# Kernel tuning notes

Hardware: AMD Instinct MI355X
Metric: run time of the kernel (lower is better)

The kernel has to match this reference:

```python
import jax, jax.numpy as jnp
import numpy as np

BUFFER_C = 1.25

def setup_inputs() -> dict:
    key = jax.random.key(0)
    k1, k2, k3 = jax.random.split(key, 3)
    T, D, E = 4096, 1024, 8
    x = jax.random.normal(k1, (T, D), dtype=jnp.float32)
    Wg = jax.random.normal(k2, (D, E), dtype=jnp.float32) / np.sqrt(D)
    bg = jnp.zeros((E,), dtype=jnp.float32)
    W = jax.random.normal(k3, (E, D, D), dtype=jnp.float32) / np.sqrt(D)
    b = jnp.zeros((E, D), dtype=jnp.float32)
    return {"x": x, "Wg": Wg, "bg": bg, "W": W, "b": b}


def reference(x, Wg, bg, W, b):
    # Top-1 (Switch-style) routing with capacity buffer, per-expert Linear,
    # prob-weighted combine, plus load-balancing aux loss.
    T, D = x.shape
    E = W.shape[0]
    capacity = int(BUFFER_C * T / E)

    logits = x @ Wg + bg                      # [T, E]
    probs = jax.nn.softmax(logits, axis=-1)   # [T, E]
    top_idx = jnp.argmax(probs, axis=-1)      # [T]
    top_prob = jnp.take_along_axis(probs, top_idx[:, None], axis=-1)[:, 0]

    onehot = jax.nn.one_hot(top_idx, E, dtype=x.dtype)       # [T, E]
    # 1-indexed position of each token within its expert's buffer
    pos = jnp.cumsum(onehot, axis=0) * onehot                # [T, E]
    dispatch = jnp.where((onehot > 0) & (pos <= capacity), 1.0, 0.0).astype(x.dtype)

    # dense dispatch/combine equivalent of the masked per-expert loop
    xe = jnp.einsum('te,td->etd', dispatch, x)               # [E, T, D]
    ye = jnp.einsum('etd,edf->etf', xe, W) + b[:, None, :]   # [E, T, D]
    y = jnp.einsum('te,etf->tf', dispatch, ye)               # [T, D] (0 for dropped)
    out = y * top_prob[:, None]

    # aux load-balance loss: E * sum_e f_e * P_e
    f = onehot.mean(axis=0)
    P = probs.mean(axis=0)
    aux_loss = E * jnp.sum(f * P)
    return out, aux_loss
```

## Files before the change

### kernel.cpp

```cpp
#include <hip/hip_runtime.h>
#include <hip/hip_bf16.h>
#include <cstdint>

#define T_TOK 4096
#define D_DIM 1024
#define E_EXP 8
#define CAP   640
#define MAXDROP 3456
#define MT    10
#define GBLK  1024
#define NSUB  32

typedef __attribute__((ext_vector_type(8))) short short8;
typedef __attribute__((ext_vector_type(4))) float f32x4;

__device__ inline unsigned short f2bf(float f) {
    uint32_t u = __float_as_uint(f);
    u += 0x7fffu + ((u >> 16) & 1u);
    return (unsigned short)(u >> 16);
}

__device__ inline void dma16(const void* g, void* l) {
    __builtin_amdgcn_global_load_lds(
        (const __attribute__((address_space(1))) unsigned int*)g,
        (__attribute__((address_space(3))) unsigned int*)l, 16, 0, 0);
}

#define WB_TILE(e, nt, kt) ((((size_t)(e) * 16 + (nt)) * 16 + (kt)) * 4096)
#define XG_TILE(e, mt, kt) ((((size_t)(e) * MT + (mt)) * 16 + (kt)) * 4096)

__global__ __launch_bounds__(256) void prep_kernel(
    const float* __restrict__ x, const float* __restrict__ Wg,
    const float* __restrict__ bg, const float* __restrict__ W,
    unsigned short* __restrict__ Wb,
    int* __restrict__ top_idx, float* __restrict__ top_prob,
    float* __restrict__ blkpart)
{
    int bid = blockIdx.x;
    int tid = threadIdx.x;

    if (bid >= GBLK) {
        int bid2 = (bid - GBLK) * 2;
        int e   = bid2 >> 8;
        int kt  = (bid2 >> 4) & 15;
        int ntA = bid2 & 15;
        int k0  = kt * 64;
        const float* Wsrc = W + (size_t)e * D_DIM * D_DIM + (size_t)k0 * D_DIM;

        int c0 = tid, c1 = tid + 256;
        int g0 = c0 >> 6, n0c = c0 & 63;
        int g1 = c1 >> 6, n1c = c1 & 63;

        #pragma unroll
        for (int half = 0; half < 2; half++) {
            int n0 = (ntA + half) * 64;
            unsigned short* dst = Wb + WB_TILE(e, ntA + half, kt);
            const float* s0 = Wsrc + (size_t)(g0 * 8) * D_DIM + n0 + n0c;
            const float* s1 = Wsrc + (size_t)(g1 * 8) * D_DIM + n0 + n1c;
            float v[8], u[8];
            #pragma unroll
            for (int z = 0; z < 8; z++) v[z] = s0[(size_t)z * D_DIM];
            #pragma unroll
            for (int z = 0; z < 8; z++) u[z] = s1[(size_t)z * D_DIM];
            short8 a, b2;
            #pragma unroll
            for (int z = 0; z < 8; z++) { a[z] = (short)f2bf(v[z]); b2[z] = (short)f2bf(u[z]); }
            *(short8*)&dst[(size_t)c0 * 8] = a;
            *(short8*)&dst[(size_t)c1 * 8] = b2;
        }
    } else {
        __shared__ float probs_sm[4][8];
        int wid  = tid >> 6;
        int lane = tid & 63;
        int t = bid * 4 + wid;

        const float* xr = x + (size_t)t * D_DIM;

        float acc[8];
        #pragma unroll
        for (int e = 0; e < 8; e++) acc[e] = 0.f;

        #pragma unroll
        for (int ii = 0; ii < 16; ii++) {
            int d = lane + 64 * ii;
            float xv = xr[d];
            const float4* wr = (const float4*)(Wg + (size_t)d * 8);
            float4 a = wr[0], bq = wr[1];
            acc[0] += xv * a.x;  acc[1] += xv * a.y;
            acc[2] += xv * a.z;  acc[3] += xv * a.w;
            acc[4] += xv * bq.x; acc[5] += xv * bq.y;
            acc[6] += xv * bq.z; acc[7] += xv * bq.w;
        }
        #pragma unroll
        for (int off = 32; off > 0; off >>= 1) {
            #pragma unroll
            for (int e = 0; e < 8; e++) acc[e] += __shfl_xor(acc[e], off, 64);
        }
        if (lane == 0) {
            float lg[8];
            #pragma unroll
            for (int e = 0; e < 8; e++) lg[e] = acc[e] + bg[e];
            float m = lg[0]; int am = 0;
            #pragma unroll
            for (int e = 1; e < 8; e++) { if (lg[e] > m) { m = lg[e]; am = e; } }
            float ex[8], s = 0.f;
            #pragma unroll
            for (int e = 0; e < 8; e++) { ex[e] = __expf(lg[e] - m); s += ex[e]; }
            float inv = 1.f / s;
            top_idx[t]  = am;
            top_prob[t] = ex[am] * inv;
            #pragma unroll
            for (int e = 0; e < 8; e++) probs_sm[wid][e] = ex[e] * inv;
        }
        __syncthreads();
        if (tid < 8) {
            float s = probs_sm[0][tid] + probs_sm[1][tid]
                    + probs_sm[2][tid] + probs_sm[3][tid];
            blkpart[(size_t)bid * 8 + tid] = s;
        }
    }
}

__global__ __launch_bounds__(1024) void scan_kernel(
    const int* __restrict__ top_idx,
    int* __restrict__ tok_list, int* __restrict__ cnt,
    const float* __restrict__ blkpart,
    float* __restrict__ out, float* __restrict__ out_aux)
{
    __shared__ int counts[64][8];
    __shared__ int excl[64][8];
    __shared__ int fulltot[8];
    __shared__ int droplist[MAXDROP];
    __shared__ int ndrop;
    __shared__ float wpart[16][8];

    int tid  = threadIdx.x;
    int wv   = tid >> 6;
    int lane = tid & 63;
    unsigned long long ltmask = (lane == 0) ? 0ull : ((~0ull) >> (64 - lane));

    if (tid == 0) ndrop = 0;

    float p[8];
    {
        const float4* bp = (const float4*)(blkpart + (size_t)tid * 8);
        float4 p0 = bp[0], p1 = bp[1];
        p[0] = p0.x; p[1] = p0.y; p[2] = p0.z; p[3] = p0.w;
        p[4] = p1.x; p[5] = p1.y; p[6] = p1.z; p[7] = p1.w;
    }

    int ecache[4];
    #pragma unroll
    for (int c = 0; c < 4; c++)
        ecache[c] = top_idx[(4 * wv + c) * 64 + lane];

    #pragma unroll
    for (int c = 0; c < 4; c++) {
        int chunk = 4 * wv + c;
        int e = ecache[c];
        #pragma unroll
        for (int q = 0; q < 8; q++) {
            unsigned long long mk = __ballot(e == q);
            int tot = __popcll(mk);
            if (lane == q) counts[chunk][q] = tot;
        }
    }
    __syncthreads();

    if (wv == 0) {
        #pragma unroll
        for (int q = 0; q < 8; q++) {
            int v = counts[lane][q];
            int orig = v;
            #pragma unroll
            for (int off = 1; off < 64; off <<= 1) {
                int n = __shfl_up(v, off, 64);
                if (lane >= off) v += n;
            }
            excl[lane][q] = v - orig;
            int total = __shfl(v, 63, 64);
            if (lane == 0) {
                fulltot[q] = total;
                cnt[q] = total < CAP ? total : CAP;
            }
        }
    }
    __syncthreads();

    #pragma unroll
    for (int c = 0; c < 4; c++) {
        int chunk = 4 * wv + c;
        int t = chunk * 64 + lane;
        int e = ecache[c];
        int pos = 0;
        #pragma unroll
        for (int q = 0; q < 8; q++) {
            unsigned long long mk = __ballot(e == q);
            if (e == q) pos = excl[chunk][q] + __popcll(mk & ltmask);
        }
        if (pos < CAP) {
            tok_list[e * CAP + pos] = t;
        } else {
            int di = atomicAdd(&ndrop, 1);
            droplist[di] = t;
        }
    }

    #pragma unroll
    for (int off = 32; off > 0; off >>= 1) {
        #pragma unroll
        for (int e = 0; e < 8; e++) p[e] += __shfl_xor(p[e], off, 64);
    }
    if (lane == 0) {
        #pragma unroll
        for (int e = 0; e < 8; e++) wpart[wv][e] = p[e];
    }
    __syncthreads();

    int nd = ndrop;
    int grp = tid >> 8;
    int col = (tid & 255) * 4;
    float4 z = {0.f, 0.f, 0.f, 0.f};
    for (int d = grp; d < nd; d += 4) {
        int row = droplist[d];
        *(float4*)&out[(size_t)row * D_DIM + col] = z;
    }

    if (tid == 0) {
        float s = 0.f;
        #pragma unroll
        for (int e = 0; e < 8; e++) {
            float Pe = 0.f;
            #pragma unroll
            for (int w = 0; w < 16; w++) Pe += wpart[w][e];
            s += ((float)fulltot[e] / (float)T_TOK) * (Pe / (float)T_TOK);
        }
        out_aux[0] = (float)E_EXP * s;
    }
}

__global__ __launch_bounds__(256) void gather_kernel(
    const float* __restrict__ x, const int* __restrict__ tok_list,
    const int* __restrict__ cnt, unsigned short* __restrict__ xg)
{
    int bid = blockIdx.x;
    int e   = bid / (MT * 16);
    int rem = bid % (MT * 16);
    int mt  = rem >> 4, kt = rem & 15;
    int count = cnt[e];
    int m0 = mt * 64;
    if (m0 >= count) return;

    int tid = threadIdx.x;
    const int* tl = tok_list + e * CAP;
    unsigned short* dst = xg + XG_TILE(e, mt, kt);

    #pragma unroll
    for (int p = 0; p < 2; p++) {
        int c = tid + 256 * p;
        int g = c >> 6, row = c & 63;
        int gm = m0 + row;
        int tok = tl[gm < count ? gm : count - 1];
        const float* src = x + (size_t)tok * D_DIM + kt * 64 + g * 8;
        float4 v0 = *(const float4*)(src);
        float4 v1 = *(const float4*)(src + 4);
        short8 v;
        v[0] = f2bf(v0.x); v[1] = f2bf(v0.y); v[2] = f2bf(v0.z); v[3] = f2bf(v0.w);
        v[4] = f2bf(v1.x); v[5] = f2bf(v1.y); v[6] = f2bf(v1.z); v[7] = f2bf(v1.w);
        *(short8*)&dst[(size_t)c * 8] = v;
    }
}

__global__ __launch_bounds__(512) void expert_gemm(
    const unsigned short* __restrict__ xg, const unsigned short* __restrict__ Wb,
    const float* __restrict__ bias,
    const int* __restrict__ tok_list, const int* __restrict__ cnt,
    const float* __restrict__ top_prob, float* __restrict__ out)
{
    int orig = blockIdx.x;
    int bid  = (orig & 7) * 40 + (orig >> 3);
    int e   = bid / 40;
    int rem = bid % 40;
    int mtb = rem >> 3, ntb = rem & 7;
    int count = cnt[e];
    int m0 = mtb * 128;
    if (m0 >= count) return;
    int n0 = ntb * 128;

    __shared__ unsigned short Ab[3][2][4][64][8];
    __shared__ unsigned short Bb[3][2][4][64][8];

    int tid  = threadIdx.x;
    int lane = tid & 63, w = tid >> 6;
    int quad = lane >> 4, l16 = lane & 15;
    int wr = w >> 2, wc = w & 3;

    const int* tl = tok_list + e * CAP;

    int  wa    = w & 3;
    int  shalf = wa >> 1;
    int  sg0   = (wa & 1) * 2;
    const unsigned short* sbase =
        (w < 4) ? (xg + XG_TILE(e, 2 * mtb + shalf, 0) + (size_t)lane * 8)
                : (Wb + WB_TILE(e, 2 * ntb + shalf, 0) + (size_t)lane * 8);

    #define STAGE(s, buf) do {                                                  \
        size_t off_ = (size_t)((s) >> 1) * 4096 + (size_t)((s) & 1) * 2048;     \
        if (w < 4) {                                                            \
            dma16(sbase + off_ + (size_t)sg0 * 512,       &Ab[buf][shalf][sg0][0][0]);     \
            dma16(sbase + off_ + (size_t)(sg0 + 1) * 512, &Ab[buf][shalf][sg0 + 1][0][0]); \
        } else {                                                                \
            dma16(sbase + off_ + (size_t)sg0 * 512,       &Bb[buf][shalf][sg0][0][0]);     \
            dma16(sbase + off_ + (size_t)(sg0 + 1) * 512, &Bb[buf][shalf][sg0 + 1][0][0]); \
        }                                                                       \
    } while (0)

    f32x4 acc[4][2];
    #pragma unroll
    for (int i = 0; i < 4; i++)
        #pragma unroll
        for (int j = 0; j < 2; j++)
            acc[i][j] = (f32x4){0.f, 0.f, 0.f, 0.f};

    STAGE(0, 0);
    STAGE(1, 1);

    #pragma unroll 1
    for (int s = 0; s < NSUB; s++) {
        if (s + 1 < NSUB) { asm volatile("s_waitcnt vmcnt(2)" ::: "memory"); }
        else              { asm volatile("s_waitcnt vmcnt(0)" ::: "memory"); }
        __builtin_amdgcn_s_barrier();
        __builtin_amdgcn_sched_barrier(0);

        int cur = s % 3;
        if (s + 2 < NSUB)
            STAGE(s + 2, (s + 2) % 3);

        short8 af[4], bf[2];
        #pragma unroll
        for (int i = 0; i < 4; i++)
            af[i] = *(const short8*)&Ab[cur][wr][quad][16 * i + l16][0];
        #pragma unroll
        for (int j = 0; j < 2; j++) {
            int cb = wc * 32 + 16 * j;
            bf[j] = *(const short8*)&Bb[cur][cb >> 6][quad][(cb & 63) + l16][0];
        }
        #pragma unroll
        for (int i = 0; i < 4; i++)
            #pragma unroll
            for (int j = 0; j < 2; j++)
                acc[i][j] = __builtin_amdgcn_mfma_f32_16x16x32_bf16(
                    af[i], bf[j], acc[i][j], 0, 0, 0);
    }
    #undef STAGE

    float bv[2];
    #pragma unroll
    for (int j = 0; j < 2; j++)
        bv[j] = bias[e * D_DIM + n0 + wc * 32 + 16 * j + l16];

    #pragma unroll
    for (int i = 0; i < 4; i++) {
        int rb = m0 + wr * 64 + 16 * i + quad * 4;
        #pragma unroll
        for (int r = 0; r < 4; r++) {
            int gm = rb + r;
            if (gm >= count) continue;
            int tok = tl[gm];
            float p = top_prob[tok];
            float* orow = out + (size_t)tok * D_DIM + n0 + wc * 32 + l16;
            #pragma unroll
            for (int j = 0; j < 2; j++)
                orow[16 * j] = (acc[i][j][r] + bv[j]) * p;
        }
    }
}

extern "C" void kernel_launch(void* const* d_in, const int* in_sizes, int n_in,
                              void* d_out, int out_size, void* d_ws, size_t ws_size,
                              hipStream_t stream) {
    const float* x  = (const float*)d_in[0];
    const float* Wg = (const float*)d_in[1];
    const float* bg = (const float*)d_in[2];
    const float* W  = (const float*)d_in[3];
    const float* b  = (const float*)d_in[4];
    float* out = (float*)d_out;

    char* ws = (char*)d_ws;
    unsigned short* Wb = (unsigned short*)(ws + 0);
    unsigned short* xg = (unsigned short*)(ws + 16777216);
    int*   top_idx  = (int*)(ws + 27262976);
    float* top_prob = (float*)(ws + 27279360);
    int*   tok_list = (int*)(ws + 27295744);
    int*   cnt      = (int*)(ws + 27316224);
    float* blkpart  = (float*)(ws + 27316256);

    hipLaunchKernelGGL(prep_kernel, dim3(GBLK + 1024), dim3(256), 0, stream,
                       x, Wg, bg, W, Wb, top_idx, top_prob, blkpart);
    hipLaunchKernelGGL(scan_kernel, dim3(1), dim3(1024), 0, stream,
                       top_idx, tok_list, cnt, blkpart, out, out + (size_t)T_TOK * D_DIM);
    hipLaunchKernelGGL(gather_kernel, dim3(E_EXP * MT * 16), dim3(256), 0, stream,
                       x, tok_list, cnt, xg);
    hipLaunchKernelGGL(expert_gemm, dim3(E_EXP * 5 * 8), dim3(512), 0, stream,
                       xg, Wb, b, tok_list, cnt, top_prob, out);
}
```

Before: 138.5 us.

## Split weight conversion across prep and scan kernels to overlap serial scan

Half of the fp32-to-bf16 weight conversion blocks move out of prep_kernel into the scan launch. Scan now runs as block 0 with 256 threads, each covering four times the chunks, while the other 512 blocks convert weights. The aim is to hide the single-block serial scan behind useful bandwidth-bound work and shorten prep. In exchange, the scan block has fewer threads and runs longer, and its dropped-row zeroing loop is now serial per row.

```diff
diff --git a/kernel.cpp b/kernel.cpp
--- a/kernel.cpp
+++ b/kernel.cpp
@@ -10,6 +10,7 @@
 #define MT    10
 #define GBLK  1024
 #define NSUB  32
+#define WHALF 512
 
 typedef __attribute__((ext_vector_type(8))) short short8;
 typedef __attribute__((ext_vector_type(4))) float f32x4;
@@ -28,6 +29,40 @@
 
 #define WB_TILE(e, nt, kt) ((((size_t)(e) * 16 + (nt)) * 16 + (kt)) * 4096)
 #define XG_TILE(e, mt, kt) ((((size_t)(e) * MT + (mt)) * 16 + (kt)) * 4096)
+
+__device__ inline void wconv_pair(const float* __restrict__ W,
+                                  unsigned short* __restrict__ Wb,
+                                  int pb, int tid)
+{
+    int bid2 = pb * 2;
+    int e   = bid2 >> 8;
+    int kt  = (bid2 >> 4) & 15;
+    int ntA = bid2 & 15;
+    int k0  = kt * 64;
+    const float* Wsrc = W + (size_t)e * D_DIM * D_DIM + (size_t)k0 * D_DIM;
+
+    int c0 = tid, c1 = tid + 256;
+    int g0 = c0 >> 6, n0c = c0 & 63;
+    int g1 = c1 >> 6, n1c = c1 & 63;
+
+    #pragma unroll
+    for (int half = 0; half < 2; half++) {
+        int n0 = (ntA + half) * 64;
+        unsigned short* dst = Wb + WB_TILE(e, ntA + half, kt);
+        const float* s0 = Wsrc + (size_t)(g0 * 8) * D_DIM + n0 + n0c;
+        const float* s1 = Wsrc + (size_t)(g1 * 8) * D_DIM + n0 + n1c;
+        float v[8], u[8];
+        #pragma unroll
+        for (int z = 0; z < 8; z++) v[z] = s0[(size_t)z * D_DIM];
+        #pragma unroll
+        for (int z = 0; z < 8; z++) u[z] = s1[(size_t)z * D_DIM];
+        short8 a, b2;
+        #pragma unroll
+        for (int z = 0; z < 8; z++) { a[z] = (short)f2bf(v[z]); b2[z] = (short)f2bf(u[z]); }
+        *(short8*)&dst[(size_t)c0 * 8] = a;
+        *(short8*)&dst[(size_t)c1 * 8] = b2;
+    }
+}
 
 __global__ __launch_bounds__(256) void prep_kernel(
     const float* __restrict__ x, const float* __restrict__ Wg,
@@ -40,34 +75,7 @@
     int tid = threadIdx.x;
 
     if (bid >= GBLK) {
-        int bid2 = (bid - GBLK) * 2;
-        int e   = bid2 >> 8;
-        int kt  = (bid2 >> 4) & 15;
-        int ntA = bid2 & 15;
-        int k0  = kt * 64;
-        const float* Wsrc = W + (size_t)e * D_DIM * D_DIM + (size_t)k0 * D_DIM;
-
-        int c0 = tid, c1 = tid + 256;
-        int g0 = c0 >> 6, n0c = c0 & 63;
-        int g1 = c1 >> 6, n1c = c1 & 63;
-
-        #pragma unroll
-        for (int half = 0; half < 2; half++) {
-            int n0 = (ntA + half) * 64;
-            unsigned short* dst = Wb + WB_TILE(e, ntA + half, kt);
-            const float* s0 = Wsrc + (size_t)(g0 * 8) * D_DIM + n0 + n0c;
-            const float* s1 = Wsrc + (size_t)(g1 * 8) * D_DIM + n0 + n1c;
-            float v[8], u[8];
-            #pragma unroll
-            for (int z = 0; z < 8; z++) v[z] = s0[(size_t)z * D_DIM];
-            #pragma unroll
-            for (int z = 0; z < 8; z++) u[z] = s1[(size_t)z * D_DIM];
-            short8 a, b2;
-            #pragma unroll
-            for (int z = 0; z < 8; z++) { a[z] = (short)f2bf(v[z]); b2[z] = (short)f2bf(u[z]); }
-            *(short8*)&dst[(size_t)c0 * 8] = a;
-            *(short8*)&dst[(size_t)c1 * 8] = b2;
-        }
+        wconv_pair(W, Wb, bid - GBLK, tid);
     } else {
         __shared__ float probs_sm[4][8];
         int wid  = tid >> 6;
@@ -121,20 +129,28 @@
     }
 }
 
-__global__ __launch_bounds__(1024) void scan_kernel(
+__global__ __launch_bounds__(256) void scan_wconv_kernel(
+    const float* __restrict__ W, unsigned short* __restrict__ Wb,
     const int* __restrict__ top_idx,
     int* __restrict__ tok_list, int* __restrict__ cnt,
     const float* __restrict__ blkpart,
     float* __restrict__ out, float* __restrict__ out_aux)
 {
+    int bid = blockIdx.x;
+    int tid = threadIdx.x;
+
+    if (bid > 0) {
+        wconv_pair(W, Wb, WHALF + bid - 1, tid);
+        return;
+    }
+
     __shared__ int counts[64][8];
     __shared__ int excl[64][8];
     __shared__ int fulltot[8];
     __shared__ int droplist[MAXDROP];
     __shared__ int ndrop;
-    __shared__ float wpart[16][8];
-
-    int tid  = threadIdx.x;
+    __shared__ float wpart[4][8];
+
     int wv   = tid >> 6;
     int lane = tid & 63;
     unsigned long long ltmask = (lane == 0) ? 0ull : ((~0ull) >> (64 - lane));
@@ -142,21 +158,24 @@
     if (tid == 0) ndrop = 0;
 
     float p[8];
-    {
-        const float4* bp = (const float4*)(blkpart + (size_t)tid * 8);
+    #pragma unroll
+    for (int e = 0; e < 8; e++) p[e] = 0.f;
+    #pragma unroll
+    for (int r = 0; r < 4; r++) {
+        const float4* bp = (const float4*)(blkpart + (size_t)(tid * 4 + r) * 8);
         float4 p0 = bp[0], p1 = bp[1];
-        p[0] = p0.x; p[1] = p0.y; p[2] = p0.z; p[3] = p0.w;
-        p[4] = p1.x; p[5] = p1.y; p[6] = p1.z; p[7] = p1.w;
-    }
-
-    int ecache[4];
-    #pragma unroll
-    for (int c = 0; c < 4; c++)
-        ecache[c] = top_idx[(4 * wv + c) * 64 + lane];
-
-    #pragma unroll
-    for (int c = 0; c < 4; c++) {
-        int chunk = 4 * wv + c;
+        p[0] += p0.x; p[1] += p0.y; p[2] += p0.z; p[3] += p0.w;
+        p[4] += p1.x; p[5] += p1.y; p[6] += p1.z; p[7] += p1.w;
+    }
+
+    int ecache[16];
+    #pragma unroll
+    for (int c = 0; c < 16; c++)
+        ecache[c] = top_idx[(wv * 16 + c) * 64 + lane];
+
+    #pragma unroll
+    for (int c = 0; c < 16; c++) {
+        int chunk = wv * 16 + c;
         int e = ecache[c];
         #pragma unroll
         for (int q = 0; q < 8; q++) {
@@ -188,8 +207,8 @@
     __syncthreads();
 
     #pragma unroll
-    for (int c = 0; c < 4; c++) {
-        int chunk = 4 * wv + c;
+    for (int c = 0; c < 16; c++) {
+        int chunk = wv * 16 + c;
         int t = chunk * 64 + lane;
         int e = ecache[c];
         int pos = 0;
@@ -218,21 +237,17 @@
     __syncthreads();
 
     int nd = ndrop;
-    int grp = tid >> 8;
-    int col = (tid & 255) * 4;
     float4 z = {0.f, 0.f, 0.f, 0.f};
-    for (int d = grp; d < nd; d += 4) {
+    for (int d = 0; d < nd; d++) {
         int row = droplist[d];
-        *(float4*)&out[(size_t)row * D_DIM + col] = z;
+        *(float4*)&out[(size_t)row * D_DIM + tid * 4] = z;
     }
 
     if (tid == 0) {
         float s = 0.f;
         #pragma unroll
         for (int e = 0; e < 8; e++) {
-            float Pe = 0.f;
-            #pragma unroll
-            for (int w = 0; w < 16; w++) Pe += wpart[w][e];
+            float Pe = wpart[0][e] + wpart[1][e] + wpart[2][e] + wpart[3][e];
             s += ((float)fulltot[e] / (float)T_TOK) * (Pe / (float)T_TOK);
         }
         out_aux[0] = (float)E_EXP * s;
@@ -395,10 +410,11 @@
     int*   cnt      = (int*)(ws + 27316224);
     float* blkpart  = (float*)(ws + 27316256);
 
-    hipLaunchKernelGGL(prep_kernel, dim3(GBLK + 1024), dim3(256), 0, stream,
+    hipLaunchKernelGGL(prep_kernel, dim3(GBLK + WHALF), dim3(256), 0, stream,
                        x, Wg, bg, W, Wb, top_idx, top_prob, blkpart);
-    hipLaunchKernelGGL(scan_kernel, dim3(1), dim3(1024), 0, stream,
-                       top_idx, tok_list, cnt, blkpart, out, out + (size_t)T_TOK * D_DIM);
+    hipLaunchKernelGGL(scan_wconv_kernel, dim3(1 + WHALF), dim3(256), 0, stream,
+                       W, Wb, top_idx, tok_list, cnt, blkpart,
+                       out, out + (size_t)T_TOK * D_DIM);
     hipLaunchKernelGGL(gather_kernel, dim3(E_EXP * MT * 16), dim3(256), 0, stream,
                        x, tok_list, cnt, xg);
     hipLaunchKernelGGL(expert_gemm, dim3(E_EXP * 5 * 8), dim3(512), 0, stream,
```

New measurement: 146.6 us. 5.9% more time.
